# Performance work log

Hardware: AMD Instinct MI355X
Metric: run time of the kernel (lower is better)

## Reference

```python
import math
import jax, jax.numpy as jnp
import numpy as np

N_HEADS = 16


def setup_inputs() -> dict:
    key = jax.random.key(0)
    qkv = jax.random.normal(key, (4, 3072, 2048), dtype=jnp.float32)
    return {"qkv": qkv}


def reference(qkv) -> jnp.ndarray:
    bs, width, length = qkv.shape
    assert width % (3 * N_HEADS) == 0
    ch = width // (3 * N_HEADS)
    # [bs*H, 3*ch, T] -> q, k, v each [bs*H, ch, T]
    qkv_r = qkv.reshape(bs * N_HEADS, 3 * ch, length)
    q, k, v = qkv_r[:, :ch], qkv_r[:, ch:2 * ch], qkv_r[:, 2 * ch:]
    scale = 1.0 / math.sqrt(math.sqrt(ch))
    # scores: [bs*H, T, T]
    weight = jnp.einsum('bct,bcs->bts', q * scale, k * scale)
    weight = jax.nn.softmax(weight.astype(jnp.float32), axis=-1).astype(weight.dtype)
    a = jnp.einsum('bts,bcs->bct', weight, v)  # [bs*H, ch, T]
    return a.reshape(bs, N_HEADS * ch, length)
```

## Files before the change

kernel.cpp:

```cpp
#include <hip/hip_runtime.h>
#include <hip/hip_bf16.h>
#include <cstdint>
#include <cstddef>

typedef short bf16x8 __attribute__((ext_vector_type(8)));
typedef float f32x4 __attribute__((ext_vector_type(4)));

#if __has_builtin(__builtin_amdgcn_exp2f)
#define EXP2F(x) __builtin_amdgcn_exp2f(x)
#else
#define EXP2F(x) exp2f(x)
#endif

#define QSCALE 0.18033688011112043f

__device__ __forceinline__ short f2bf(float f) {
  union { __hip_bfloat16 b; short s; } u;
  u.b = __float2bfloat16(f);
  return u.s;
}

__device__ __forceinline__ unsigned int packbf2(float a, float b) {
  union { unsigned short u[2]; unsigned int w; } x;
  x.u[0] = (unsigned short)f2bf(a);
  x.u[1] = (unsigned short)f2bf(b);
  return x.w;
}

__global__ __launch_bounds__(256, 4) void qkv_prep_kernel(
    const float* __restrict__ qkv, short* __restrict__ Kt,
    short* __restrict__ Vb) {
  const int bh = blockIdx.x >> 5;
  const int s0 = (blockIdx.x & 31) << 6;
  const int tid = threadIdx.x;
  const int row = tid >> 2;
  const int part = tid & 3;
  __shared__ float lds[64 * 65];

  const size_t qb = (size_t)bh * (192 * 2048);

  {
    const float* src = qkv + qb + (size_t)(64 + row) * 2048 + s0 + part * 16;
#pragma unroll
    for (int k4 = 0; k4 < 4; ++k4) {
      float4 v = ((const float4*)src)[k4];
      float* p = &lds[row * 65 + part * 16 + k4 * 4];
      p[0] = v.x; p[1] = v.y; p[2] = v.z; p[3] = v.w;
    }
  }
  __syncthreads();
  {
    bf16x8 o0, o1;
#pragma unroll
    for (int k = 0; k < 8; ++k) o0[k] = f2bf(lds[(part * 16 + k) * 65 + row]);
#pragma unroll
    for (int k = 0; k < 8; ++k) o1[k] = f2bf(lds[(part * 16 + 8 + k) * 65 + row]);
    short* dst = Kt + ((size_t)bh * 2048 + s0 + row) * 64 + part * 16;
    *(bf16x8*)dst = o0;
    *(bf16x8*)(dst + 8) = o1;
  }
  {
    const float* src = qkv + qb + (size_t)(128 + row) * 2048 + s0 + part * 16;
    float a[16];
#pragma unroll
    for (int k4 = 0; k4 < 4; ++k4) {
      float4 v = ((const float4*)src)[k4];
      a[k4 * 4 + 0] = v.x; a[k4 * 4 + 1] = v.y;
      a[k4 * 4 + 2] = v.z; a[k4 * 4 + 3] = v.w;
    }
    bf16x8 o0, o1;
#pragma unroll
    for (int k = 0; k < 8; ++k) { o0[k] = f2bf(a[k]); o1[k] = f2bf(a[8 + k]); }
    short* dst = Vb + ((size_t)bh * 64 + row) * 2048 + s0 + part * 16;
    *(bf16x8*)dst = o0;
    *(bf16x8*)(dst + 8) = o1;
  }
}

__global__ __launch_bounds__(256, 3) void attn32_kernel(
    const float* __restrict__ qkv, const short* __restrict__ Kt,
    const short* __restrict__ Vb, float* __restrict__ out) {
  const int bid = blockIdx.x;
  const int vid = (bid & 7) * 128 + (bid >> 3);
  const int bh = vid >> 4;
  const int tblk = vid & 15;
  const int tid = threadIdx.x;
  const int wv = tid >> 6;
  const int lane = tid & 63;
  const int lo = lane & 15;
  const int g = lane >> 4;
  const int t0 = tblk * 128 + wv * 32;

  __shared__ __align__(16) char smem[49152];
  char* const Pls = smem + 32768 + wv * 4096;

  const size_t qb = (size_t)bh * (192 * 2048);
  bf16x8 qf[2][2];
#pragma unroll
  for (int nt = 0; nt < 2; ++nt) {
    const int t = t0 + nt * 16 + lo;
#pragma unroll
    for (int ks = 0; ks < 2; ++ks) {
#pragma unroll
      for (int j = 0; j < 8; ++j) {
        const int c = ks * 32 + g * 8 + j;
        qf[nt][ks][j] = f2bf(qkv[qb + (size_t)c * 2048 + t] * QSCALE);
      }
    }
  }

  f32x4 acc[4][2];
#pragma unroll
  for (int ct = 0; ct < 4; ++ct)
#pragma unroll
    for (int nt = 0; nt < 2; ++nt) acc[ct][nt] = f32x4{0.f, 0.f, 0.f, 0.f};

  float mrun[2] = {-1e30f, -1e30f};
  float lsum[2] = {0.f, 0.f};

  const int srow = tid >> 3;
  const int col8 = tid & 7;
  const short* kptr = Kt + (size_t)bh * (2048 * 64) + (size_t)srow * 64 + col8 * 8;
  const short* vptr = Vb + ((size_t)bh * 64 + srow) * 2048 + col8 * 8;
  const int sdst = srow * 128 + ((col8 * 16) ^ ((srow & 7) * 16));

  bf16x8 kq[2], vq[2];
#pragma unroll
  for (int q = 0; q < 2; ++q) {
    kq[q] = *(const bf16x8*)(kptr + (size_t)(q * 32) * 64);
    vq[q] = *(const bf16x8*)(vptr + (size_t)(q * 32) * 2048);
  }

  for (int ch = 0; ch < 32; ++ch) {
    char* const Kls = smem + (ch & 1) * 16384;
    char* const Vls = Kls + 8192;

#pragma unroll
    for (int q = 0; q < 2; ++q) {
      *(bf16x8*)(Kls + sdst + q * 4096) = kq[q];
      *(bf16x8*)(Vls + sdst + q * 4096) = vq[q];
    }
    __syncthreads();

    const int s0n = (ch < 31 ? ch + 1 : 31) * 64;
    bf16x8 kn[2], vn[2];
#pragma unroll
    for (int q = 0; q < 2; ++q) {
      kn[q] = *(const bf16x8*)(kptr + (size_t)(s0n + q * 32) * 64);
      vn[q] = *(const bf16x8*)(vptr + (size_t)(q * 32) * 2048 + s0n);
    }

    f32x4 lg[4][2];
#pragma unroll
    for (int mt = 0; mt < 4; ++mt) {
#pragma unroll
      for (int nt = 0; nt < 2; ++nt) lg[mt][nt] = f32x4{0.f, 0.f, 0.f, 0.f};
      const int sr = mt * 16 + lo;
#pragma unroll
      for (int ks = 0; ks < 2; ++ks) {
        const bf16x8 ka = *(const bf16x8*)(
            Kls + sr * 128 + ((ks * 64 + g * 16) ^ ((sr & 7) * 16)));
#pragma unroll
        for (int nt = 0; nt < 2; ++nt)
          lg[mt][nt] = __builtin_amdgcn_mfma_f32_16x16x32_bf16(
              ka, qf[nt][ks], lg[mt][nt], 0, 0, 0);
      }
    }

#pragma unroll
    for (int nt = 0; nt < 2; ++nt) {
      float cm = fmaxf(fmaxf(lg[0][nt][0], lg[0][nt][1]),
                       fmaxf(lg[0][nt][2], lg[0][nt][3]));
#pragma unroll
      for (int mt = 1; mt < 4; ++mt)
        cm = fmaxf(cm, fmaxf(fmaxf(lg[mt][nt][0], lg[mt][nt][1]),
                             fmaxf(lg[mt][nt][2], lg[mt][nt][3])));
      cm = fmaxf(cm, __shfl_xor(cm, 16));
      cm = fmaxf(cm, __shfl_xor(cm, 32));
      if (!__all(cm <= mrun[nt] + 8.0f)) {
        const float nm = fmaxf(mrun[nt], cm);
        const float fac = EXP2F(mrun[nt] - nm);
        mrun[nt] = nm;
        lsum[nt] *= fac;
#pragma unroll
        for (int ct = 0; ct < 4; ++ct) acc[ct][nt] *= fac;
      }
    }

#pragma unroll
    for (int sh = 0; sh < 2; ++sh) {
#pragma unroll
      for (int mh = 0; mh < 2; ++mh) {
        const int mt = sh * 2 + mh;
#pragma unroll
        for (int nt = 0; nt < 2; ++nt) {
          const int t = nt * 16 + lo;
          f32x4 p;
#pragma unroll
          for (int r = 0; r < 4; ++r) p[r] = EXP2F(lg[mt][nt][r] - mrun[nt]);
          lsum[nt] += (p[0] + p[1]) + (p[2] + p[3]);
          uint2 w;
          w.x = packbf2(p[0], p[1]);
          w.y = packbf2(p[2], p[3]);
          *(uint2*)(Pls + t * 128 + ((mh * 32 + g * 8) ^ ((t & 7) * 16))) = w;
        }
      }
      bf16x8 pb[2];
#pragma unroll
      for (int nt = 0; nt < 2; ++nt) {
        const int t = nt * 16 + lo;
        pb[nt] = *(const bf16x8*)(Pls + t * 128 + ((g * 16) ^ ((t & 7) * 16)));
      }
#pragma unroll
      for (int ct = 0; ct < 4; ++ct) {
        const int cr = ct * 16 + lo;
        const bf16x8 va = *(const bf16x8*)(
            Vls + cr * 128 + ((sh * 64 + g * 16) ^ ((cr & 7) * 16)));
#pragma unroll
        for (int nt = 0; nt < 2; ++nt)
          acc[ct][nt] = __builtin_amdgcn_mfma_f32_16x16x32_bf16(
              va, pb[nt], acc[ct][nt], 0, 0, 0);
      }
    }

#pragma unroll
    for (int q = 0; q < 2; ++q) { kq[q] = kn[q]; vq[q] = vn[q]; }
  }

#pragma unroll
  for (int nt = 0; nt < 2; ++nt) {
    float s = lsum[nt];
    s += __shfl_xor(s, 16);
    s += __shfl_xor(s, 32);
    const float inv = 1.0f / s;
    const int t = t0 + nt * 16 + lo;
#pragma unroll
    for (int ct = 0; ct < 4; ++ct) {
#pragma unroll
      for (int r = 0; r < 4; ++r) {
        const int c = ct * 16 + g * 4 + r;
        out[((size_t)bh * 64 + c) * 2048 + t] = acc[ct][nt][r] * inv;
      }
    }
  }
}

extern "C" void kernel_launch(void* const* d_in, const int* in_sizes, int n_in,
                              void* d_out, int out_size, void* d_ws,
                              size_t ws_size, hipStream_t stream) {
  (void)in_sizes; (void)n_in; (void)out_size;
  const float* qkv = (const float*)d_in[0];
  float* out = (float*)d_out;
  const size_t kv_elems = (size_t)64 * 2048 * 64;
  if (ws_size < kv_elems * 2 * sizeof(short)) return;
  short* Kt = (short*)d_ws;
  short* Vb = Kt + kv_elems;
  hipLaunchKernelGGL(qkv_prep_kernel, dim3(2048), dim3(256), 0, stream,
                     qkv, Kt, Vb);
  hipLaunchKernelGGL(attn32_kernel, dim3(1024), dim3(256), 0, stream,
                     qkv, Kt, Vb, out);
}
```

Measured before the change: 128.2 us.

## Switch attention to 32x32x16 MFMA and pass P through registers

Replaces the 16x16x32 bf16 MFMA tiling with 32x32x16 MFMAs. Each wave now owns 32 query columns in a single tile, which gives one running max and sum per lane. The probability matrix is repacked into MFMA operand layout with cross-half-wave shuffles instead of a per-wave LDS round-trip, shrinking shared memory from 48 KB to 32 KB. The float-to-bf16 packing becomes a cheap round-half-up bit trick in place of the library conversion, which slightly changes rounding behaviour.

```diff
diff --git a/kernel.cpp b/kernel.cpp
--- a/kernel.cpp
+++ b/kernel.cpp
@@ -5,6 +5,7 @@
 
 typedef short bf16x8 __attribute__((ext_vector_type(8)));
 typedef float f32x4 __attribute__((ext_vector_type(4)));
+typedef float f32x16 __attribute__((ext_vector_type(16)));
 
 #if __has_builtin(__builtin_amdgcn_exp2f)
 #define EXP2F(x) __builtin_amdgcn_exp2f(x)
@@ -20,11 +21,12 @@
   return u.s;
 }
 
-__device__ __forceinline__ unsigned int packbf2(float a, float b) {
-  union { unsigned short u[2]; unsigned int w; } x;
-  x.u[0] = (unsigned short)f2bf(a);
-  x.u[1] = (unsigned short)f2bf(b);
-  return x.w;
+__device__ __forceinline__ unsigned int bitsf(float f) {
+  union { float f; unsigned int u; } x; x.f = f; return x.u;
+}
+
+__device__ __forceinline__ unsigned int pkbf(float a, float b) {
+  return ((bitsf(a) + 0x8000u) >> 16) | ((bitsf(b) + 0x8000u) & 0xFFFF0000u);
 }
 
 __global__ __launch_bounds__(256, 4) void qkv_prep_kernel(
@@ -87,36 +89,31 @@
   const int tid = threadIdx.x;
   const int wv = tid >> 6;
   const int lane = tid & 63;
-  const int lo = lane & 15;
-  const int g = lane >> 4;
-  const int t0 = tblk * 128 + wv * 32;
-
-  __shared__ __align__(16) char smem[49152];
-  char* const Pls = smem + 32768 + wv * 4096;
+  const int tl = lane & 31;
+  const int hi = lane >> 5;
+  const int t0w = tblk * 128 + wv * 32;
+
+  __shared__ __align__(16) char smem[32768];
 
   const size_t qb = (size_t)bh * (192 * 2048);
-  bf16x8 qf[2][2];
-#pragma unroll
-  for (int nt = 0; nt < 2; ++nt) {
-    const int t = t0 + nt * 16 + lo;
-#pragma unroll
-    for (int ks = 0; ks < 2; ++ks) {
-#pragma unroll
-      for (int j = 0; j < 8; ++j) {
-        const int c = ks * 32 + g * 8 + j;
-        qf[nt][ks][j] = f2bf(qkv[qb + (size_t)c * 2048 + t] * QSCALE);
-      }
-    }
-  }
-
-  f32x4 acc[4][2];
-#pragma unroll
-  for (int ct = 0; ct < 4; ++ct)
-#pragma unroll
-    for (int nt = 0; nt < 2; ++nt) acc[ct][nt] = f32x4{0.f, 0.f, 0.f, 0.f};
-
-  float mrun[2] = {-1e30f, -1e30f};
-  float lsum[2] = {0.f, 0.f};
+  bf16x8 qf[4];
+#pragma unroll
+  for (int kc = 0; kc < 4; ++kc) {
+#pragma unroll
+    for (int j = 0; j < 8; ++j) {
+      const int c = kc * 16 + hi * 8 + j;
+      qf[kc][j] = f2bf(qkv[qb + (size_t)c * 2048 + t0w + tl] * QSCALE);
+    }
+  }
+
+  f32x16 acc[2];
+#pragma unroll
+  for (int cb = 0; cb < 2; ++cb)
+#pragma unroll
+    for (int r = 0; r < 16; ++r) acc[cb][r] = 0.f;
+
+  float mrun = -1e30f;
+  float lsum = 0.f;
 
   const int srow = tid >> 3;
   const int col8 = tid & 7;
@@ -150,76 +147,77 @@
       vn[q] = *(const bf16x8*)(vptr + (size_t)(q * 32) * 2048 + s0n);
     }
 
-    f32x4 lg[4][2];
-#pragma unroll
-    for (int mt = 0; mt < 4; ++mt) {
-#pragma unroll
-      for (int nt = 0; nt < 2; ++nt) lg[mt][nt] = f32x4{0.f, 0.f, 0.f, 0.f};
-      const int sr = mt * 16 + lo;
-#pragma unroll
-      for (int ks = 0; ks < 2; ++ks) {
-        const bf16x8 ka = *(const bf16x8*)(
-            Kls + sr * 128 + ((ks * 64 + g * 16) ^ ((sr & 7) * 16)));
-#pragma unroll
-        for (int nt = 0; nt < 2; ++nt)
-          lg[mt][nt] = __builtin_amdgcn_mfma_f32_16x16x32_bf16(
-              ka, qf[nt][ks], lg[mt][nt], 0, 0, 0);
-      }
-    }
-
-#pragma unroll
-    for (int nt = 0; nt < 2; ++nt) {
-      float cm = fmaxf(fmaxf(lg[0][nt][0], lg[0][nt][1]),
-                       fmaxf(lg[0][nt][2], lg[0][nt][3]));
-#pragma unroll
-      for (int mt = 1; mt < 4; ++mt)
-        cm = fmaxf(cm, fmaxf(fmaxf(lg[mt][nt][0], lg[mt][nt][1]),
-                             fmaxf(lg[mt][nt][2], lg[mt][nt][3])));
-      cm = fmaxf(cm, __shfl_xor(cm, 16));
-      cm = fmaxf(cm, __shfl_xor(cm, 32));
-      if (!__all(cm <= mrun[nt] + 8.0f)) {
-        const float nm = fmaxf(mrun[nt], cm);
-        const float fac = EXP2F(mrun[nt] - nm);
-        mrun[nt] = nm;
-        lsum[nt] *= fac;
-#pragma unroll
-        for (int ct = 0; ct < 4; ++ct) acc[ct][nt] *= fac;
-      }
-    }
-
-#pragma unroll
-    for (int sh = 0; sh < 2; ++sh) {
-#pragma unroll
-      for (int mh = 0; mh < 2; ++mh) {
-        const int mt = sh * 2 + mh;
-#pragma unroll
-        for (int nt = 0; nt < 2; ++nt) {
-          const int t = nt * 16 + lo;
-          f32x4 p;
-#pragma unroll
-          for (int r = 0; r < 4; ++r) p[r] = EXP2F(lg[mt][nt][r] - mrun[nt]);
-          lsum[nt] += (p[0] + p[1]) + (p[2] + p[3]);
-          uint2 w;
-          w.x = packbf2(p[0], p[1]);
-          w.y = packbf2(p[2], p[3]);
-          *(uint2*)(Pls + t * 128 + ((mh * 32 + g * 8) ^ ((t & 7) * 16))) = w;
-        }
-      }
-      bf16x8 pb[2];
-#pragma unroll
-      for (int nt = 0; nt < 2; ++nt) {
-        const int t = nt * 16 + lo;
-        pb[nt] = *(const bf16x8*)(Pls + t * 128 + ((g * 16) ^ ((t & 7) * 16)));
-      }
-#pragma unroll
-      for (int ct = 0; ct < 4; ++ct) {
-        const int cr = ct * 16 + lo;
-        const bf16x8 va = *(const bf16x8*)(
-            Vls + cr * 128 + ((sh * 64 + g * 16) ^ ((cr & 7) * 16)));
-#pragma unroll
-        for (int nt = 0; nt < 2; ++nt)
-          acc[ct][nt] = __builtin_amdgcn_mfma_f32_16x16x32_bf16(
-              va, pb[nt], acc[ct][nt], 0, 0, 0);
+    f32x16 lg[2];
+#pragma unroll
+    for (int st = 0; st < 2; ++st) {
+#pragma unroll
+      for (int r = 0; r < 16; ++r) lg[st][r] = 0.f;
+      const int row = st * 32 + tl;
+      const int rsw = (row & 7) * 16;
+#pragma unroll
+      for (int kc = 0; kc < 4; ++kc) {
+        const bf16x8 ka =
+            *(const bf16x8*)(Kls + row * 128 + ((kc * 32 + hi * 16) ^ rsw));
+        lg[st] = __builtin_amdgcn_mfma_f32_32x32x16_bf16(ka, qf[kc], lg[st],
+                                                         0, 0, 0);
+      }
+    }
+
+    float cm = fmaxf(lg[0][0], lg[1][0]);
+#pragma unroll
+    for (int r = 1; r < 16; ++r) cm = fmaxf(cm, fmaxf(lg[0][r], lg[1][r]));
+    cm = fmaxf(cm, __shfl_xor(cm, 32));
+    if (!__all(cm <= mrun + 8.0f)) {
+      const float nm = fmaxf(mrun, cm);
+      const float fac = EXP2F(mrun - nm);
+      mrun = nm;
+      lsum *= fac;
+#pragma unroll
+      for (int cb = 0; cb < 2; ++cb)
+#pragma unroll
+        for (int r = 0; r < 16; ++r) acc[cb][r] *= fac;
+    }
+
+#pragma unroll
+    for (int st = 0; st < 2; ++st)
+#pragma unroll
+      for (int r = 0; r < 16; ++r) {
+        lg[st][r] = EXP2F(lg[st][r] - mrun);
+        lsum += lg[st][r];
+      }
+
+    bf16x8 pa[4];
+#pragma unroll
+    for (int st = 0; st < 2; ++st) {
+#pragma unroll
+      for (int kl = 0; kl < 2; ++kl) {
+        const unsigned int p0a = pkbf(lg[st][8 * kl + 0], lg[st][8 * kl + 1]);
+        const unsigned int p0b = pkbf(lg[st][8 * kl + 2], lg[st][8 * kl + 3]);
+        const unsigned int p1a = pkbf(lg[st][8 * kl + 4], lg[st][8 * kl + 5]);
+        const unsigned int p1b = pkbf(lg[st][8 * kl + 6], lg[st][8 * kl + 7]);
+        const unsigned int sa = hi ? p0a : p1a;
+        const unsigned int sb = hi ? p0b : p1b;
+        const unsigned int ra = __shfl_xor(sa, 32);
+        const unsigned int rb = __shfl_xor(sb, 32);
+        union { unsigned int w[4]; bf16x8 v; } u;
+        u.w[0] = hi ? ra : p0a;
+        u.w[1] = hi ? rb : p0b;
+        u.w[2] = hi ? p1a : ra;
+        u.w[3] = hi ? p1b : rb;
+        pa[st * 2 + kl] = u.v;
+      }
+    }
+
+#pragma unroll
+    for (int cb = 0; cb < 2; ++cb) {
+      const int rowv = cb * 32 + tl;
+      const int vsw = (rowv & 7) * 16;
+#pragma unroll
+      for (int ks = 0; ks < 4; ++ks) {
+        const bf16x8 vb =
+            *(const bf16x8*)(Vls + rowv * 128 + ((ks * 32 + hi * 16) ^ vsw));
+        acc[cb] = __builtin_amdgcn_mfma_f32_32x32x16_bf16(vb, pa[ks], acc[cb],
+                                                          0, 0, 0);
       }
     }
 
@@ -227,20 +225,14 @@
     for (int q = 0; q < 2; ++q) { kq[q] = kn[q]; vq[q] = vn[q]; }
   }
 
-#pragma unroll
-  for (int nt = 0; nt < 2; ++nt) {
-    float s = lsum[nt];
-    s += __shfl_xor(s, 16);
-    s += __shfl_xor(s, 32);
-    const float inv = 1.0f / s;
-    const int t = t0 + nt * 16 + lo;
-#pragma unroll
-    for (int ct = 0; ct < 4; ++ct) {
-#pragma unroll
-      for (int r = 0; r < 4; ++r) {
-        const int c = ct * 16 + g * 4 + r;
-        out[((size_t)bh * 64 + c) * 2048 + t] = acc[ct][nt][r] * inv;
-      }
+  const float ls = lsum + __shfl_xor(lsum, 32);
+  const float inv = 1.0f / ls;
+#pragma unroll
+  for (int cb = 0; cb < 2; ++cb) {
+#pragma unroll
+    for (int r = 0; r < 16; ++r) {
+      const int c = cb * 32 + (r & 3) + 8 * (r >> 2) + 4 * hi;
+      out[((size_t)bh * 64 + c) * 2048 + t0w + tl] = acc[cb][r] * inv;
     }
   }
 }
```

After: 129.5 us. No clear change (+1.0%).
